# Kernel optimization log

Hardware: AMD Instinct MI355X
Metric: run time of the kernel (lower is better)

Reference implementation:

```python
import jax, jax.numpy as jnp
import numpy as np

KERNEL_MUL = 2.0
KERNEL_NUM = 5
EPS = 1e-3


def setup_inputs() -> dict:
    key = jax.random.key(0)
    k1, k2 = jax.random.split(key)
    source = jax.random.normal(k1, (2048, 512), dtype=jnp.float32)
    target = jax.random.normal(k2, (2048, 512), dtype=jnp.float32)
    beta = jnp.ones((KERNEL_NUM,), dtype=jnp.float32) / KERNEL_NUM
    return {"source": source, "target": target, "beta": beta}


def _sq_dists(total):
    # squared Euclidean pairwise distances, (N, N), clamped >= 0 (matches cdist(p=2)**2)
    sq = jnp.sum(total * total, axis=-1)
    d = sq[:, None] + sq[None, :] - 2.0 * (total @ total.T)
    return jnp.maximum(d, 0.0)


def _project_simplex(v):
    m = v.shape[0]
    mu = -jnp.sort(-v)                      # descending
    cs = jnp.cumsum(mu)
    ar = jnp.arange(1, m + 1, dtype=v.dtype)
    cond = mu - (cs - 1.0) / ar > 0
    idx = jnp.where(cond, jnp.arange(m), -1)
    rho = jnp.where(jnp.any(cond), jnp.max(idx), 0)
    theta = (cs[rho] - 1.0) / (rho + 1).astype(v.dtype)
    p = jnp.maximum(v - theta, 0.0)
    return p / (p.sum() + 1e-12)


def _update_beta(source, target, beta):
    # Batched version of the per-pair quad-kernel loop in _update_beta.
    Ns, D = source.shape
    Nt = target.shape[0]
    P = min(Ns // 2, Nt // 2)  # num_effective_pairs (static)
    s = source[: 2 * P].reshape(P, 2, D)
    t = target[: 2 * P].reshape(P, 2, D)
    quad = jnp.concatenate([s, t], axis=1)              # (P, 4, D) -> [s1, s2, t1, t2]
    diff = quad[:, :, None, :] - quad[:, None, :, :]
    sq = jnp.sum(diff * diff, axis=-1)                  # (P, 4, 4)
    offdiag = ~np.eye(4, dtype=bool)
    bw = jnp.median(sq[:, offdiag], axis=1) + 1e-6      # per-pair median of nonzero dists
    bw = bw / (KERNEL_MUL ** (KERNEL_NUM // 2))
    bws = bw[:, None] * (KERNEL_MUL ** jnp.arange(KERNEL_NUM, dtype=bw.dtype))[None, :]
    K = jnp.exp(-sq[:, None, :, :] / bws[:, :, None, None])   # (P, 5, 4, 4)
    g = K[:, :, 0, 1] + K[:, :, 2, 3] - K[:, :, 0, 2] - K[:, :, 1, 3]  # (P, 5)
    gm = jnp.mean(g, axis=0)
    Q = (g.T @ g) / P - jnp.outer(gm, gm) + EPS * jnp.eye(KERNEL_NUM, dtype=g.dtype)
    # projected gradient descent on the simplex (lr=1, max_iter=100, tol=1e-6)
    def cond_fn(st):
        _, _, i, conv = st
        return (i < 100) & (~conv)
    def body_fn(st):
        b, _, i, _ = st
        proj = _project_simplex(b - Q @ b)
        conv = jnp.linalg.norm(proj - b) < 1e-6
        return (proj, proj, i + 1, conv)
    _, proj, _, _ = jax.lax.while_loop(
        cond_fn, body_fn, (beta, beta, jnp.int32(0), jnp.array(False)))
    return proj


def _forward(source, target, beta):
    beta_new = _update_beta(jax.lax.stop_gradient(source),
                            jax.lax.stop_gradient(target), beta)
    Ns = source.shape[0]
    total = jnp.concatenate([source, target], axis=0)   # (N, D)
    N = total.shape[0]
    sq = _sq_dists(total)                               # (N, N)
    offdiag = ~np.eye(N, dtype=bool)
    bw = jnp.median(sq[offdiag]) + 1e-6
    bw = bw / (KERNEL_MUL ** (KERNEL_NUM // 2))
    bws = bw * (KERNEL_MUL ** jnp.arange(KERNEL_NUM, dtype=sq.dtype))  # (5,)
    Ks = jnp.exp(-sq[None, :, :] / bws[:, None, None])  # (5, N, N)
    joint = jnp.einsum('k,kij->ij', beta_new, Ks)
    XX = joint[:Ns, :Ns]
    YY = joint[Ns:, Ns:]
    XY = joint[:Ns, Ns:]
    n = XX.shape[0]
    m = YY.shape[0]
    term_XX = (jnp.sum(XX) - jnp.trace(XX)) / (n * (n - 1))
    term_YY = (jnp.sum(YY) - jnp.trace(YY)) / (m * (m - 1))
    term_XY = jnp.sum(XY) / (n * m)
    loss = term_XX + term_YY - 2.0 * term_XY
    return jnp.maximum(loss, 0.0)


def reference(source, target, beta):
    return _forward(source, target, beta)
```

## Files before the change

kernel.cpp:

```cpp
#include <hip/hip_runtime.h>
#include <math.h>

#define NT 4096
#define NS 2048
#define DDIM 512
#define KN 5
#define NTILES 528

typedef __bf16 bf16x8 __attribute__((ext_vector_type(8)));
typedef float f32x4 __attribute__((ext_vector_type(4)));
typedef unsigned short u16x8 __attribute__((ext_vector_type(8)));

static __device__ inline unsigned short f2bf(float x) {
    unsigned u = __float_as_uint(x);
    unsigned r = (u + 0x7fffu + ((u >> 16) & 1u)) >> 16;
    return (unsigned short)r;
}
static __device__ inline float bf2f(unsigned short h) {
    return __uint_as_float(((unsigned)h) << 16);
}

static __device__ inline void tri_map(int b, int& bx, int& by) {
    int x = (int)((sqrtf(8.0f * (float)b + 1.0f) - 1.0f) * 0.5f);
    while ((x + 1) * (x + 2) / 2 <= b) ++x;
    while (x * (x + 1) / 2 > b) --x;
    bx = x;
    by = b - x * (x + 1) / 2;
}

static __device__ void beta_solve(const float* __restrict__ g,
                                  const float* __restrict__ beta_in,
                                  float* __restrict__ beta_out)
{
    int lane = threadIdx.x;
    float gs[KN] = {0, 0, 0, 0, 0};
    float gg[15];
    #pragma unroll
    for (int i = 0; i < 15; ++i) gg[i] = 0.0f;
    for (int p = lane; p < 1024; p += 64) {
        float gv[KN];
        #pragma unroll
        for (int k = 0; k < KN; ++k) gv[k] = g[(size_t)p * KN + k];
        int idx = 0;
        #pragma unroll
        for (int a2 = 0; a2 < KN; ++a2) {
            gs[a2] += gv[a2];
            #pragma unroll
            for (int b2 = a2; b2 < KN; ++b2) gg[idx++] += gv[a2] * gv[b2];
        }
    }
    #pragma unroll
    for (int m = 32; m > 0; m >>= 1) {
        #pragma unroll
        for (int k = 0; k < KN; ++k) gs[k] += __shfl_xor(gs[k], m);
        #pragma unroll
        for (int i = 0; i < 15; ++i) gg[i] += __shfl_xor(gg[i], m);
    }
    if (lane != 0) return;

    float Q[KN][KN], gm[KN];
    #pragma unroll
    for (int k = 0; k < KN; ++k) gm[k] = gs[k] * (1.0f / 1024.0f);
    int idx = 0;
    #pragma unroll
    for (int a2 = 0; a2 < KN; ++a2)
        #pragma unroll
        for (int b2 = a2; b2 < KN; ++b2) {
            float qv = gg[idx++] * (1.0f / 1024.0f) - gm[a2] * gm[b2];
            Q[a2][b2] = qv; Q[b2][a2] = qv;
        }
    #pragma unroll
    for (int k = 0; k < KN; ++k) Q[k][k] += 0.001f;

    float b[KN], proj[KN];
    #pragma unroll
    for (int k = 0; k < KN; ++k) { b[k] = beta_in[k]; proj[k] = b[k]; }
    for (int it = 0; it < 100; ++it) {
        float v[KN];
        #pragma unroll
        for (int a2 = 0; a2 < KN; ++a2) {
            float qb = Q[a2][0] * b[0] + Q[a2][1] * b[1] + Q[a2][2] * b[2]
                     + Q[a2][3] * b[3] + Q[a2][4] * b[4];
            v[a2] = b[a2] - qb;
        }
        float mu0 = v[0], mu1 = v[1], mu2 = v[2], mu3 = v[3], mu4 = v[4];
#define CMPSW(x, y) { float hi_ = fmaxf(x, y); float lo_ = fminf(x, y); x = hi_; y = lo_; }
        CMPSW(mu0, mu1) CMPSW(mu3, mu4) CMPSW(mu2, mu4) CMPSW(mu2, mu3)
        CMPSW(mu0, mu3) CMPSW(mu0, mu2) CMPSW(mu1, mu4) CMPSW(mu1, mu3) CMPSW(mu1, mu2)
#undef CMPSW
        float cs0 = mu0, cs1 = cs0 + mu1, cs2 = cs1 + mu2, cs3 = cs2 + mu3, cs4 = cs3 + mu4;
        bool c1 = mu1 * 2.0f > cs1 - 1.0f;
        bool c2 = mu2 * 3.0f > cs2 - 1.0f;
        bool c3 = mu3 * 4.0f > cs3 - 1.0f;
        bool c4 = mu4 * 5.0f > cs4 - 1.0f;
        float csSel = cs0, rcpSel = 1.0f;
        if (c1) { csSel = cs1; rcpSel = 0.5f; }
        if (c2) { csSel = cs2; rcpSel = (1.0f / 3.0f); }
        if (c3) { csSel = cs3; rcpSel = 0.25f; }
        if (c4) { csSel = cs4; rcpSel = 0.2f; }
        float theta = (csSel - 1.0f) * rcpSel;
        float ssum = 0.0f;
        #pragma unroll
        for (int k = 0; k < KN; ++k) { proj[k] = fmaxf(v[k] - theta, 0.0f); ssum += proj[k]; }
        float invs = 1.0f / (ssum + 1e-12f);
        float nd = 0.0f;
        #pragma unroll
        for (int k = 0; k < KN; ++k) {
            proj[k] *= invs;
            float dd = proj[k] - b[k];
            nd += dd * dd;
            b[k] = proj[k];
        }
        if (nd < 1e-12f) break;
    }
    #pragma unroll
    for (int k = 0; k < KN; ++k) beta_out[k] = proj[k];
}

__global__ __launch_bounds__(256) void k_prep2(const float* __restrict__ S,
                                               const float* __restrict__ T,
                                               unsigned short* __restrict__ Hi,
                                               unsigned short* __restrict__ Lo,
                                               float* __restrict__ norms,
                                               float* __restrict__ g,
                                               unsigned* __restrict__ hists,
                                               unsigned* __restrict__ sel)
{
    if (blockIdx.x < 44) hists[blockIdx.x * 256 + threadIdx.x] = 0;
    if (blockIdx.x == 50 && threadIdx.x == 0) {
        sel[0] = 0u; sel[1] = 8386559u;
        sel[2] = 0u; sel[3] = 8386560u;
    }
    int p = blockIdx.x * 4 + (threadIdx.x >> 6);
    int l = threadIdx.x & 63;
    const float* r0 = S + (size_t)(2 * p) * DDIM;
    const float* r1 = r0 + DDIM;
    const float* r2 = T + (size_t)(2 * p) * DDIM;
    const float* r3 = r2 + DDIM;
    float a[8], b[8], c[8], d[8];
    *(float4*)&a[0] = *(const float4*)(r0 + l * 8); *(float4*)&a[4] = *(const float4*)(r0 + l * 8 + 4);
    *(float4*)&b[0] = *(const float4*)(r1 + l * 8); *(float4*)&b[4] = *(const float4*)(r1 + l * 8 + 4);
    *(float4*)&c[0] = *(const float4*)(r2 + l * 8); *(float4*)&c[4] = *(const float4*)(r2 + l * 8 + 4);
    *(float4*)&d[0] = *(const float4*)(r3 + l * 8); *(float4*)&d[4] = *(const float4*)(r3 + l * 8 + 4);

    float n0 = 0, n1 = 0, n2 = 0, n3 = 0;
    float s01 = 0, s23 = 0, s02 = 0, s13 = 0, s03 = 0, s12 = 0;
    u16x8 h0, l0, h1, l1, h2, l2, h3, l3;
    #pragma unroll
    for (int k = 0; k < 8; ++k) {
        float va = a[k], vb = b[k], vc = c[k], vd = d[k];
        n0 += va * va; n1 += vb * vb; n2 += vc * vc; n3 += vd * vd;
        float t01 = va - vb, t23 = vc - vd, t02 = va - vc, t13 = vb - vd;
        s01 += t01*t01; s23 += t23*t23; s02 += t02*t02; s13 += t13*t13;
        float t03 = va - vd, t12 = vb - vc;
        s03 += t03*t03; s12 += t12*t12;
        unsigned short hh;
        hh = f2bf(va); h0[k] = hh; l0[k] = f2bf(va - bf2f(hh));
        hh = f2bf(vb); h1[k] = hh; l1[k] = f2bf(vb - bf2f(hh));
        hh = f2bf(vc); h2[k] = hh; l2[k] = f2bf(vc - bf2f(hh));
        hh = f2bf(vd); h3[k] = hh; l3[k] = f2bf(vd - bf2f(hh));
    }
    size_t g0 = (size_t)(2 * p) * DDIM + l * 8;
    size_t g1 = g0 + DDIM;
    size_t g2 = (size_t)(NS + 2 * p) * DDIM + l * 8;
    size_t g3 = g2 + DDIM;
    *(u16x8*)&Hi[g0] = h0; *(u16x8*)&Lo[g0] = l0;
    *(u16x8*)&Hi[g1] = h1; *(u16x8*)&Lo[g1] = l1;
    *(u16x8*)&Hi[g2] = h2; *(u16x8*)&Lo[g2] = l2;
    *(u16x8*)&Hi[g3] = h3; *(u16x8*)&Lo[g3] = l3;

    #pragma unroll
    for (int m = 32; m > 0; m >>= 1) {
        n0 += __shfl_xor(n0, m); n1 += __shfl_xor(n1, m);
        n2 += __shfl_xor(n2, m); n3 += __shfl_xor(n3, m);
        s01 += __shfl_xor(s01, m); s23 += __shfl_xor(s23, m);
        s02 += __shfl_xor(s02, m); s13 += __shfl_xor(s13, m);
        s03 += __shfl_xor(s03, m); s12 += __shfl_xor(s12, m);
    }
    if (l == 0) {
        norms[2 * p] = n0; norms[2 * p + 1] = n1;
        norms[NS + 2 * p] = n2; norms[NS + 2 * p + 1] = n3;
        float v[6] = { s01, s02, s03, s12, s13, s23 };
        for (int i = 0; i < 5; ++i)
            for (int j = 0; j < 5 - i; ++j)
                if (v[j] > v[j + 1]) { float t = v[j]; v[j] = v[j + 1]; v[j + 1] = t; }
        float med = 0.5f * (v[2] + v[3]);
        float bw = (med + 1e-6f) * 0.25f;
        #pragma unroll
        for (int k = 0; k < KN; ++k) {
            float inv = 1.0f / (bw * (float)(1 << k));
            g[(size_t)p * KN + k] = expf(-s01 * inv) + expf(-s23 * inv)
                                  - expf(-s02 * inv) - expf(-s13 * inv);
        }
    }
}

__global__ __launch_bounds__(256) void k_dist_mfma(const unsigned short* __restrict__ Hi,
                                                   const unsigned short* __restrict__ Lo,
                                                   const float* __restrict__ norms,
                                                   float* __restrict__ D,
                                                   const float* __restrict__ g,
                                                   const float* __restrict__ beta_in,
                                                   float* __restrict__ beta_out)
{
    __shared__ __align__(16) unsigned short sA[2][2][128][32];
    __shared__ __align__(16) unsigned short sB[2][2][128][32];

    if (blockIdx.x == 0) {
        if (threadIdx.x < 64) beta_solve(g, beta_in, beta_out);
        return;
    }

    int bb = blockIdx.x - 1;
    int swz = (bb & 7) * 66 + (bb >> 3);
    int bx, by;
    tri_map(swz, bx, by);
    const int m0 = by * 128, n0 = bx * 128;

    const int tid = threadIdx.x;
    const int w = tid >> 6, l = tid & 63;
    const int wr = w >> 1, wc = w & 1;

    const int chunk = (l & 3) ^ ((((l >> 2) & 3) + ((l >> 4) & 3)) & 3);
    const size_t gA0 = (size_t)(m0 + w * 16 + (l >> 2)) * DDIM + chunk * 8;
    const size_t gA1 = gA0 + (size_t)64 * DDIM;
    const size_t gB0 = (size_t)(n0 + w * 16 + (l >> 2)) * DDIM + chunk * 8;
    const size_t gB1 = gB0 + (size_t)64 * DDIM;
    const unsigned w1024 = w * 1024;

#define GLD(dst, srcptr, goff)                                                      \
    __builtin_amdgcn_global_load_lds(                                               \
        (const __attribute__((address_space(1))) unsigned*)((srcptr) + (goff)),     \
        (__attribute__((address_space(3))) unsigned*)((char*)(dst) + w1024), 16, 0, 0)
#define STAGE(buf, kk)                                  \
    do {                                                \
        GLD(&sA[buf][0][0][0],  Hi, gA0 + (kk));        \
        GLD(&sA[buf][0][64][0], Hi, gA1 + (kk));        \
        GLD(&sA[buf][1][0][0],  Lo, gA0 + (kk));        \
        GLD(&sA[buf][1][64][0], Lo, gA1 + (kk));        \
        GLD(&sB[buf][0][0][0],  Hi, gB0 + (kk));        \
        GLD(&sB[buf][0][64][0], Hi, gB1 + (kk));        \
        GLD(&sB[buf][1][0][0],  Lo, gB0 + (kk));        \
        GLD(&sB[buf][1][64][0], Lo, gB1 + (kk));        \
    } while (0)

    f32x4 acc[4][4] = {};
    const int q = l >> 4;
    const int fr = ((l & 3) + ((l >> 2) & 3)) & 3;
    const unsigned soff = ((unsigned)(q ^ fr)) << 4;
    const unsigned rowbA = (wr * 64 + (l & 15)) * 64 + soff;
    const unsigned rowbB = (wc * 64 + (l & 15)) * 64 + soff;

    STAGE(0, 0);
    __syncthreads();

    #pragma unroll 2
    for (int t = 0; t < 16; ++t) {
        const int cur = t & 1;
        if (t < 15) STAGE(cur ^ 1, (t + 1) * 32);

        bf16x8 ah[4], al[4], bh[4], bl[4];
        #pragma unroll
        for (int m = 0; m < 4; ++m) {
            ah[m] = *(const bf16x8*)((const char*)&sA[cur][0][0][0] + rowbA + m * 1024);
            al[m] = *(const bf16x8*)((const char*)&sA[cur][1][0][0] + rowbA + m * 1024);
        }
        #pragma unroll
        for (int n = 0; n < 4; ++n) {
            bh[n] = *(const bf16x8*)((const char*)&sB[cur][0][0][0] + rowbB + n * 1024);
            bl[n] = *(const bf16x8*)((const char*)&sB[cur][1][0][0] + rowbB + n * 1024);
        }
        #pragma unroll
        for (int m = 0; m < 4; ++m)
            #pragma unroll
            for (int n = 0; n < 4; ++n) {
                acc[m][n] = __builtin_amdgcn_mfma_f32_16x16x32_bf16(bh[n], ah[m], acc[m][n], 0, 0, 0);
                acc[m][n] = __builtin_amdgcn_mfma_f32_16x16x32_bf16(bl[n], ah[m], acc[m][n], 0, 0, 0);
                acc[m][n] = __builtin_amdgcn_mfma_f32_16x16x32_bf16(bh[n], al[m], acc[m][n], 0, 0, 0);
            }
        __syncthreads();
    }
#undef STAGE
#undef GLD

    float* rowbuf = (float*)&sA[0][0][0][0] + w * 1024;
    const int rr = l & 15;
    #pragma unroll
    for (int m = 0; m < 4; ++m) {
        float nrm = norms[m0 + wr * 64 + m * 16 + rr];
        #pragma unroll
        for (int n = 0; n < 4; ++n) {
            int cb = n0 + wc * 64 + n * 16 + (q << 2);
            float4 ncv = *(const float4*)&norms[cb];
            f32x4 a = acc[m][n];
            float4 o;
            o.x = fmaxf(nrm + ncv.x - 2.0f * a[0], 0.0f);
            o.y = fmaxf(nrm + ncv.y - 2.0f * a[1], 0.0f);
            o.z = fmaxf(nrm + ncv.z - 2.0f * a[2], 0.0f);
            o.w = fmaxf(nrm + ncv.w - 2.0f * a[3], 0.0f);
            int ch = (n * 4 + q) ^ (rr & 7);
            *(float4*)(rowbuf + rr * 64 + ch * 4) = o;
        }
        #pragma unroll
        for (int s = 0; s < 4; ++s) {
            int row = s * 4 + q;
            int ch = (l & 15) ^ (row & 7);
            float4 v = *(const float4*)(rowbuf + row * 64 + ch * 4);
            *(float4*)&D[(size_t)(m0 + wr * 64 + m * 16 + row) * NT + n0 + wc * 64 + (l & 15) * 4] = v;
        }
    }
}

__global__ __launch_bounds__(256) void k_hist0_tri(const float* __restrict__ D,
                                                   unsigned* __restrict__ gH)
{
    __shared__ unsigned h[1024];
    for (int i = threadIdx.x; i < 1024; i += 256) h[i] = 0;
    int bx, by;
    tri_map(blockIdx.x, bx, by);
    int m0 = by * 128, n0 = bx * 128;
    unsigned wt = (bx != by) ? 2u : 1u;
    __syncthreads();
    for (int v = threadIdx.x; v < 4096; v += 256) {
        int r = m0 + (v >> 5);
        int c0 = n0 + (v & 31) * 4;
        float4 dv = *(const float4*)&D[(size_t)r * NT + c0];
        const float* dd = (const float*)&dv;
        unsigned pb = __float_as_uint(dd[0]) >> 22;
        unsigned pc = (r == c0) ? 0u : wt;
        #pragma unroll
        for (int j = 1; j < 4; ++j) {
            unsigned bj = __float_as_uint(dd[j]) >> 22;
            unsigned cj = (r == c0 + j) ? 0u : wt;
            if (bj == pb) pc += cj;
            else {
                if (pc) atomicAdd(&h[pb], pc);
                pb = bj; pc = cj;
            }
        }
        if (pc) atomicAdd(&h[pb], pc);
    }
    __syncthreads();
    for (int i = threadIdx.x; i < 1024; i += 256) {
        unsigned c = h[i];
        if (c) atomicAdd(&gH[i], c);
    }
}

__global__ __launch_bounds__(64) void k_scan0(const unsigned* __restrict__ hL0,
                                              unsigned* __restrict__ sel)
{
    int lane = threadIdx.x;
    for (int t = 0; t < 2; ++t) {
        unsigned r = sel[t * 2 + 1];
        unsigned s = 0;
        for (int i = 0; i < 16; ++i) s += hL0[lane * 16 + i];
        unsigned x = s;
        #pragma unroll
        for (int off = 1; off < 64; off <<= 1) {
            unsigned y = __shfl_up(x, off);
            if (lane >= off) x += y;
        }
        unsigned base = x - s;
        bool has = (r >= base) && (r < base + s);
        unsigned long long mm = __ballot(has);
        int leader = __ffsll(mm) - 1;
        unsigned bin = 0, cb = 0;
        if (lane == leader) {
            unsigned cc = base;
            for (int i = 0; i < 16; ++i) {
                unsigned hv = hL0[lane * 16 + i];
                if (r < cc + hv) { bin = lane * 16 + i; cb = cc; break; }
                cc += hv;
            }
        }
        bin = __shfl(bin, leader);
        cb = __shfl(cb, leader);
        if (lane == 0) {
            sel[t * 2 + 0] = bin;
            sel[t * 2 + 1] = r - cb;
        }
    }
}

template<int LEVEL>
__global__ __launch_bounds__(256) void k_hist_tri(const float* __restrict__ D,
                                                  const unsigned* __restrict__ sel,
                                                  unsigned* __restrict__ gA,
                                                  unsigned* __restrict__ gB)
{
    constexpr int NB = (LEVEL == 2) ? 4096 : 1024;
    __shared__ unsigned lha[NB];
    __shared__ unsigned lhb[NB];
    for (int i = threadIdx.x; i < NB; i += 256) { lha[i] = 0; lhb[i] = 0; }
    unsigned pA = sel[0], pB = sel[2];
    int bx, by;
    tri_map(blockIdx.x, bx, by);
    int m0 = by * 128, n0 = bx * 128;
    unsigned wt = (bx != by) ? 2u : 1u;
    __syncthreads();
    for (int v = threadIdx.x; v < 4096; v += 256) {
        int r = m0 + (v >> 5);
        int c0 = n0 + (v & 31) * 4;
        float4 dv = *(const float4*)&D[(size_t)r * NT + c0];
        const float* dd = (const float*)&dv;
        #pragma unroll
        for (int j = 0; j < 4; ++j) {
            if (r == c0 + j) continue;
            unsigned key = __float_as_uint(dd[j]);
            if constexpr (LEVEL == 1) {
                if ((key >> 22) == pA) atomicAdd(&lha[(key >> 12) & 1023], wt);
                if ((key >> 22) == pB) atomicAdd(&lhb[(key >> 12) & 1023], wt);
            } else {
                if ((key >> 12) == pA) atomicAdd(&lha[key & 4095], wt);
                if ((key >> 12) == pB) atomicAdd(&lhb[key & 4095], wt);
            }
        }
    }
    __syncthreads();
    for (int i = threadIdx.x; i < NB; i += 256) {
        unsigned ca = lha[i];
        if (ca) atomicAdd(&gA[i], ca);
        unsigned cb = lhb[i];
        if (cb) atomicAdd(&gB[i], cb);
    }
}

template<int LEVEL>
__global__ __launch_bounds__(64) void k_scan(const unsigned* __restrict__ hA,
                                             const unsigned* __restrict__ hB,
                                             unsigned* __restrict__ sel,
                                             float* __restrict__ params)
{
    constexpr int NB = (LEVEL == 2) ? 4096 : 1024;
    constexpr int C = NB / 64;
    int lane = threadIdx.x;
    for (int t = 0; t < 2; ++t) {
        const unsigned* h = (t == 0 ? hA : hB);
        unsigned r = sel[t * 2 + 1];
        unsigned s = 0;
        for (int i = 0; i < C; ++i) s += h[lane * C + i];
        unsigned x = s;
        #pragma unroll
        for (int off = 1; off < 64; off <<= 1) {
            unsigned y = __shfl_up(x, off);
            if (lane >= off) x += y;
        }
        unsigned base = x - s;
        bool has = (r >= base) && (r < base + s);
        unsigned long long mm = __ballot(has);
        int leader = __ffsll(mm) - 1;
        unsigned bin = 0, cb = 0;
        if (lane == leader) {
            unsigned cc = base;
            for (int i = 0; i < C; ++i) {
                unsigned hv = h[lane * C + i];
                if (r < cc + hv) { bin = lane * C + i; cb = cc; break; }
                cc += hv;
            }
        }
        bin = __shfl(bin, leader);
        cb = __shfl(cb, leader);
        if (lane == 0) {
            if (LEVEL == 1) sel[t * 2 + 0] = (sel[t * 2 + 0] << 10) | bin;
            else            sel[4 + t]     = (sel[t * 2 + 0] << 12) | bin;
            sel[t * 2 + 1] = r - cb;
        }
    }
    if (LEVEL == 2 && lane == 0) {
        float vA = __uint_as_float(sel[4]);
        float vB = __uint_as_float(sel[5]);
        float med = 0.5f * (vA + vB);
        float bw = (med + 1e-6f) * 0.25f;
        #pragma unroll
        for (int k = 0; k < KN; ++k) params[k] = 1.0f / (bw * (float)(1 << k));
    }
}

__global__ __launch_bounds__(256) void k_wsum_tri(const float* __restrict__ D,
                                                  const float* __restrict__ params,
                                                  const float* __restrict__ beta,
                                                  double* __restrict__ partials)
{
    float i0 = params[0], i1 = params[1], i2 = params[2], i3 = params[3], i4 = params[4];
    float b0 = beta[0], b1 = beta[1], b2 = beta[2], b3 = beta[3], b4 = beta[4];
    const double wDiag = 1.0 / ((double)NS * (NS - 1));
    const double wOff = -1.0 / ((double)NS * NS);
    int bx, by;
    tri_map(blockIdx.x, bx, by);
    int m0 = by * 128, n0 = bx * 128;
    double wt = (bx != by) ? 2.0 : 1.0;
    double acc = 0.0;
    for (int v = threadIdx.x; v < 4096; v += 256) {
        int r = m0 + (v >> 5);
        int c0 = n0 + (v & 31) * 4;
        float4 dv = *(const float4*)&D[(size_t)r * NT + c0];
        const float* dd = (const float*)&dv;
        #pragma unroll
        for (int j = 0; j < 4; ++j) {
            int c = c0 + j;
            if (r == c) continue;
            float sq = dd[j];
            float val = b0 * __expf(-sq * i0) + b1 * __expf(-sq * i1) + b2 * __expf(-sq * i2)
                      + b3 * __expf(-sq * i3) + b4 * __expf(-sq * i4);
            bool same = (r < NS) == (c < NS);
            acc += (same ? wDiag : wOff) * (double)val;
        }
    }
    acc *= wt;
    __shared__ double red[256];
    red[threadIdx.x] = acc;
    __syncthreads();
    for (int off = 128; off > 0; off >>= 1) {
        if (threadIdx.x < off) red[threadIdx.x] += red[threadIdx.x + off];
        __syncthreads();
    }
    if (threadIdx.x == 0) partials[blockIdx.x] = red[0];
}

__global__ __launch_bounds__(256) void k_final(const double* __restrict__ partials,
                                               float* __restrict__ out, int count)
{
    double acc = 0;
    for (int i = threadIdx.x; i < count; i += 256) acc += partials[i];
    __shared__ double red[256];
    red[threadIdx.x] = acc;
    __syncthreads();
    for (int off = 128; off > 0; off >>= 1) {
        if (threadIdx.x < off) red[threadIdx.x] += red[threadIdx.x + off];
        __syncthreads();
    }
    if (threadIdx.x == 0) out[0] = (float)fmax(red[0], 0.0);
}

extern "C" void kernel_launch(void* const* d_in, const int* in_sizes, int n_in,
                              void* d_out, int out_size, void* d_ws, size_t ws_size,
                              hipStream_t stream)
{
    const float* S = (const float*)d_in[0];
    const float* T = (const float*)d_in[1];
    const float* beta = (const float*)d_in[2];
    float* out = (float*)d_out;

    float* D = (float*)d_ws;
    unsigned short* Hi = (unsigned short*)(D + (size_t)NT * NT);
    unsigned short* Lo = Hi + (size_t)NT * DDIM;
    float* norms = (float*)(Lo + (size_t)NT * DDIM);
    float* g = norms + NT;
    float* beta2 = g + 1024 * KN;
    float* params = beta2 + 8;
    unsigned* sel = (unsigned*)(params + 8);
    unsigned* hists = sel + 16;
    unsigned* hL0 = hists;
    unsigned* hL1A = hL0 + 1024;
    unsigned* hL1B = hL1A + 1024;
    unsigned* hL2A = hL1B + 1024;
    unsigned* hL2B = hL2A + 4096;
    double* partials = (double*)(hists + 11264);

    k_prep2<<<dim3(256), dim3(256), 0, stream>>>(S, T, Hi, Lo, norms, g, hists, sel);
    k_dist_mfma<<<dim3(NTILES + 1), dim3(256), 0, stream>>>(Hi, Lo, norms, D, g, beta, beta2);
    k_hist0_tri<<<dim3(NTILES), dim3(256), 0, stream>>>(D, hL0);
    k_scan0<<<dim3(1), dim3(64), 0, stream>>>(hL0, sel);
    k_hist_tri<1><<<dim3(NTILES), dim3(256), 0, stream>>>(D, sel, hL1A, hL1B);
    k_scan<1><<<dim3(1), dim3(64), 0, stream>>>(hL1A, hL1B, sel, params);
    k_hist_tri<2><<<dim3(NTILES), dim3(256), 0, stream>>>(D, sel, hL2A, hL2B);
    k_scan<2><<<dim3(1), dim3(64), 0, stream>>>(hL2A, hL2B, sel, params);
    k_wsum_tri<<<dim3(NTILES), dim3(256), 0, stream>>>(D, params, beta2, partials);
    k_final<<<dim3(1), dim3(256), 0, stream>>>(partials, out, NTILES);
}
```

Before: 151.7 us.

## Enlarge distance GEMM tiles to 256x128 to raise operand reuse

The MFMA distance kernel now computes 256x128 output tiles (4 warps, each 64x128) instead of 128x128, cutting the block count from 528 to 272 over the upper triangle. Each loaded B fragment is reused across twice as many rows, and the epilogue reads norms from an LDS cache. Diagonal blocks skip storing the lower half. The cost is doubled accumulators per thread (launch_bounds 256,1), which lowers occupancy and register headroom, and fewer blocks for 256 CUs.

Result: slower. 174.7 us (+15.2%).

```diff
diff --git a/kernel.cpp b/kernel.cpp
--- a/kernel.cpp
+++ b/kernel.cpp
@@ -6,6 +6,7 @@
 #define DDIM 512
 #define KN 5
 #define NTILES 528
+#define NDBLK 272
 
 typedef __bf16 bf16x8 __attribute__((ext_vector_type(8)));
 typedef float f32x4 __attribute__((ext_vector_type(4)));
@@ -195,15 +196,15 @@
     }
 }
 
-__global__ __launch_bounds__(256) void k_dist_mfma(const unsigned short* __restrict__ Hi,
-                                                   const unsigned short* __restrict__ Lo,
-                                                   const float* __restrict__ norms,
-                                                   float* __restrict__ D,
-                                                   const float* __restrict__ g,
-                                                   const float* __restrict__ beta_in,
-                                                   float* __restrict__ beta_out)
-{
-    __shared__ __align__(16) unsigned short sA[2][2][128][32];
+__global__ __launch_bounds__(256, 1) void k_dist_mfma(const unsigned short* __restrict__ Hi,
+                                                      const unsigned short* __restrict__ Lo,
+                                                      const float* __restrict__ norms,
+                                                      float* __restrict__ D,
+                                                      const float* __restrict__ g,
+                                                      const float* __restrict__ beta_in,
+                                                      float* __restrict__ beta_out)
+{
+    __shared__ __align__(16) unsigned short sA[2][2][256][32];
     __shared__ __align__(16) unsigned short sB[2][2][128][32];
 
     if (blockIdx.x == 0) {
@@ -212,101 +213,122 @@
     }
 
     int bb = blockIdx.x - 1;
-    int swz = (bb & 7) * 66 + (bb >> 3);
-    int bx, by;
-    tri_map(swz, bx, by);
-    const int m0 = by * 128, n0 = bx * 128;
+    int swz = (bb & 7) * 34 + (bb >> 3);
+    int t2 = swz, R = 0;
+    while (t2 >= 32 - 2 * R) { t2 -= 32 - 2 * R; ++R; }
+    const int C = 2 * R + t2;
+    const int m0 = R * 256, n0 = C * 128;
+    const bool diag = (C == 2 * R);
 
     const int tid = threadIdx.x;
     const int w = tid >> 6, l = tid & 63;
-    const int wr = w >> 1, wc = w & 1;
-
-    const int chunk = (l & 3) ^ ((((l >> 2) & 3) + ((l >> 4) & 3)) & 3);
-    const size_t gA0 = (size_t)(m0 + w * 16 + (l >> 2)) * DDIM + chunk * 8;
-    const size_t gA1 = gA0 + (size_t)64 * DDIM;
-    const size_t gB0 = (size_t)(n0 + w * 16 + (l >> 2)) * DDIM + chunk * 8;
-    const size_t gB1 = gB0 + (size_t)64 * DDIM;
-    const unsigned w1024 = w * 1024;
+
+    const int chunk = (tid & 3) ^ ((((tid >> 2) & 3) + ((tid >> 4) & 3)) & 3);
+    const int srow = tid >> 2;
+    size_t gA[4], gB[2];
+    #pragma unroll
+    for (int rb = 0; rb < 4; ++rb) gA[rb] = (size_t)(m0 + rb * 64 + srow) * DDIM + chunk * 8;
+    #pragma unroll
+    for (int rb = 0; rb < 2; ++rb) gB[rb] = (size_t)(n0 + rb * 64 + srow) * DDIM + chunk * 8;
+    const unsigned wbase = w * 1024;
 
 #define GLD(dst, srcptr, goff)                                                      \
     __builtin_amdgcn_global_load_lds(                                               \
         (const __attribute__((address_space(1))) unsigned*)((srcptr) + (goff)),     \
-        (__attribute__((address_space(3))) unsigned*)((char*)(dst) + w1024), 16, 0, 0)
-#define STAGE(buf, kk)                                  \
-    do {                                                \
-        GLD(&sA[buf][0][0][0],  Hi, gA0 + (kk));        \
-        GLD(&sA[buf][0][64][0], Hi, gA1 + (kk));        \
-        GLD(&sA[buf][1][0][0],  Lo, gA0 + (kk));        \
-        GLD(&sA[buf][1][64][0], Lo, gA1 + (kk));        \
-        GLD(&sB[buf][0][0][0],  Hi, gB0 + (kk));        \
-        GLD(&sB[buf][0][64][0], Hi, gB1 + (kk));        \
-        GLD(&sB[buf][1][0][0],  Lo, gB0 + (kk));        \
-        GLD(&sB[buf][1][64][0], Lo, gB1 + (kk));        \
+        (__attribute__((address_space(3))) unsigned*)((char*)(dst) + wbase), 16, 0, 0)
+#define STAGE(buf, kk)                                       \
+    do {                                                     \
+        GLD(&sA[buf][0][0][0],   Hi, gA[0] + (kk));          \
+        GLD(&sA[buf][0][64][0],  Hi, gA[1] + (kk));          \
+        GLD(&sA[buf][0][128][0], Hi, gA[2] + (kk));          \
+        GLD(&sA[buf][0][192][0], Hi, gA[3] + (kk));          \
+        GLD(&sA[buf][1][0][0],   Lo, gA[0] + (kk));          \
+        GLD(&sA[buf][1][64][0],  Lo, gA[1] + (kk));          \
+        GLD(&sA[buf][1][128][0], Lo, gA[2] + (kk));          \
+        GLD(&sA[buf][1][192][0], Lo, gA[3] + (kk));          \
+        GLD(&sB[buf][0][0][0],   Hi, gB[0] + (kk));          \
+        GLD(&sB[buf][0][64][0],  Hi, gB[1] + (kk));          \
+        GLD(&sB[buf][1][0][0],   Lo, gB[0] + (kk));          \
+        GLD(&sB[buf][1][64][0],  Lo, gB[1] + (kk));          \
     } while (0)
 
-    f32x4 acc[4][4] = {};
+    f32x4 acc[4][8] = {};
     const int q = l >> 4;
     const int fr = ((l & 3) + ((l >> 2) & 3)) & 3;
     const unsigned soff = ((unsigned)(q ^ fr)) << 4;
-    const unsigned rowbA = (wr * 64 + (l & 15)) * 64 + soff;
-    const unsigned rowbB = (wc * 64 + (l & 15)) * 64 + soff;
+    const unsigned rowA = (w * 64 + (l & 15)) * 64 + soff;
+    const unsigned rowB = (l & 15) * 64 + soff;
 
     STAGE(0, 0);
     __syncthreads();
 
-    #pragma unroll 2
     for (int t = 0; t < 16; ++t) {
         const int cur = t & 1;
         if (t < 15) STAGE(cur ^ 1, (t + 1) * 32);
 
-        bf16x8 ah[4], al[4], bh[4], bl[4];
+        bf16x8 ah[4], al[4];
         #pragma unroll
         for (int m = 0; m < 4; ++m) {
-            ah[m] = *(const bf16x8*)((const char*)&sA[cur][0][0][0] + rowbA + m * 1024);
-            al[m] = *(const bf16x8*)((const char*)&sA[cur][1][0][0] + rowbA + m * 1024);
-        }
-        #pragma unroll
-        for (int n = 0; n < 4; ++n) {
-            bh[n] = *(const bf16x8*)((const char*)&sB[cur][0][0][0] + rowbB + n * 1024);
-            bl[n] = *(const bf16x8*)((const char*)&sB[cur][1][0][0] + rowbB + n * 1024);
-        }
-        #pragma unroll
-        for (int m = 0; m < 4; ++m)
+            ah[m] = *(const bf16x8*)((const char*)&sA[cur][0][0][0] + rowA + m * 1024);
+            al[m] = *(const bf16x8*)((const char*)&sA[cur][1][0][0] + rowA + m * 1024);
+        }
+        #pragma unroll
+        for (int half = 0; half < 2; ++half) {
+            bf16x8 bh[4], bl[4];
             #pragma unroll
             for (int n = 0; n < 4; ++n) {
-                acc[m][n] = __builtin_amdgcn_mfma_f32_16x16x32_bf16(bh[n], ah[m], acc[m][n], 0, 0, 0);
-                acc[m][n] = __builtin_amdgcn_mfma_f32_16x16x32_bf16(bl[n], ah[m], acc[m][n], 0, 0, 0);
-                acc[m][n] = __builtin_amdgcn_mfma_f32_16x16x32_bf16(bh[n], al[m], acc[m][n], 0, 0, 0);
+                bh[n] = *(const bf16x8*)((const char*)&sB[cur][0][0][0] + rowB + (half * 4 + n) * 1024);
+                bl[n] = *(const bf16x8*)((const char*)&sB[cur][1][0][0] + rowB + (half * 4 + n) * 1024);
             }
+            #pragma unroll
+            for (int m = 0; m < 4; ++m)
+                #pragma unroll
+                for (int n = 0; n < 4; ++n) {
+                    int nn = half * 4 + n;
+                    acc[m][nn] = __builtin_amdgcn_mfma_f32_16x16x32_bf16(bh[n], ah[m], acc[m][nn], 0, 0, 0);
+                    acc[m][nn] = __builtin_amdgcn_mfma_f32_16x16x32_bf16(bl[n], ah[m], acc[m][nn], 0, 0, 0);
+                    acc[m][nn] = __builtin_amdgcn_mfma_f32_16x16x32_bf16(bh[n], al[m], acc[m][nn], 0, 0, 0);
+                }
+        }
         __syncthreads();
     }
 #undef STAGE
 #undef GLD
 
-    float* rowbuf = (float*)&sA[0][0][0][0] + w * 1024;
+    float* ncache = (float*)&sB[0][0][0][0];
+    ncache[tid] = norms[m0 + tid];
+    if (tid < 128) ncache[256 + tid] = norms[n0 + tid];
+    __syncthreads();
+
+    if (diag && w >= 2) return;
+
+    float* rowbuf = (float*)&sA[0][0][0][0] + w * 2048;
     const int rr = l & 15;
     #pragma unroll
     for (int m = 0; m < 4; ++m) {
-        float nrm = norms[m0 + wr * 64 + m * 16 + rr];
-        #pragma unroll
-        for (int n = 0; n < 4; ++n) {
-            int cb = n0 + wc * 64 + n * 16 + (q << 2);
-            float4 ncv = *(const float4*)&norms[cb];
+        float nrm = ncache[w * 64 + m * 16 + rr];
+        #pragma unroll
+        for (int n = 0; n < 8; ++n) {
+            float4 ncv = *(const float4*)&ncache[256 + n * 16 + (q << 2)];
             f32x4 a = acc[m][n];
             float4 o;
             o.x = fmaxf(nrm + ncv.x - 2.0f * a[0], 0.0f);
             o.y = fmaxf(nrm + ncv.y - 2.0f * a[1], 0.0f);
             o.z = fmaxf(nrm + ncv.z - 2.0f * a[2], 0.0f);
             o.w = fmaxf(nrm + ncv.w - 2.0f * a[3], 0.0f);
-            int ch = (n * 4 + q) ^ (rr & 7);
-            *(float4*)(rowbuf + rr * 64 + ch * 4) = o;
+            int cw = (n * 4 + q) ^ (rr & 7);
+            *(float4*)(rowbuf + rr * 128 + cw * 4) = o;
         }
         #pragma unroll
         for (int s = 0; s < 4; ++s) {
             int row = s * 4 + q;
-            int ch = (l & 15) ^ (row & 7);
-            float4 v = *(const float4*)(rowbuf + row * 64 + ch * 4);
-            *(float4*)&D[(size_t)(m0 + wr * 64 + m * 16 + row) * NT + n0 + wc * 64 + (l & 15) * 4] = v;
+            #pragma unroll
+            for (int h = 0; h < 2; ++h) {
+                int c = h * 16 + (l & 15);
+                int cr = c ^ (row & 7);
+                float4 v = *(const float4*)(rowbuf + row * 128 + cr * 4);
+                *(float4*)&D[(size_t)(m0 + w * 64 + m * 16 + row) * NT + n0 + c * 4] = v;
+            }
         }
     }
 }
@@ -552,14 +574,14 @@
     unsigned* sel = (unsigned*)(params + 8);
     unsigned* hists = sel + 16;
     unsigned* hL0 = hists;
-    unsigned* hL1A = hL0 + 1024;
-    unsigned* hL1B = hL1A + 1024;
-    unsigned* hL2A = hL1B + 1024;
-    unsigned* hL2B = hL2A + 4096;
+    unsigned* hL1A = hists + 1024;
+    unsigned* hL1B = hists + 2048;
+    unsigned* hL2A = hists + 3072;
+    unsigned* hL2B = hists + 7168;
     double* partials = (double*)(hists + 11264);
 
     k_prep2<<<dim3(256), dim3(256), 0, stream>>>(S, T, Hi, Lo, norms, g, hists, sel);
-    k_dist_mfma<<<dim3(NTILES + 1), dim3(256), 0, stream>>>(Hi, Lo, norms, D, g, beta, beta2);
+    k_dist_mfma<<<dim3(NDBLK + 1), dim3(256), 0, stream>>>(Hi, Lo, norms, D, g, beta, beta2);
     k_hist0_tri<<<dim3(NTILES), dim3(256), 0, stream>>>(D, hL0);
     k_scan0<<<dim3(1), dim3(64), 0, stream>>>(hL0, sel);
     k_hist_tri<1><<<dim3(NTILES), dim3(256), 0, stream>>>(D, sel, hL1A, hL1B);
```

## Fuse level-0 histogram into distance GEMM epilogue and final reduction into wsum

Applied to the files above, without the earlier changes.

Builds the first radix-select histogram inside the distance kernel's epilogue, using per-wave shared-memory histograms fed from the values just written. This removes a separate full pass over the distance matrix. It also folds the final partial-sum reduction into the weighted-sum kernel with a last-block atomic ticket, removing one launch. In exchange the GEMM epilogue gets extra LDS atomics and shared-memory reuse, and the ticket counter now has to be zeroed by the prep kernel.

New measurement: 152.6 us. Within noise of the previous version (+0.6%).

```diff
diff --git a/kernel.cpp b/kernel.cpp
--- a/kernel.cpp
+++ b/kernel.cpp
@@ -126,7 +126,7 @@
                                                unsigned* __restrict__ hists,
                                                unsigned* __restrict__ sel)
 {
-    if (blockIdx.x < 44) hists[blockIdx.x * 256 + threadIdx.x] = 0;
+    if (blockIdx.x < 45) hists[blockIdx.x * 256 + threadIdx.x] = 0;
     if (blockIdx.x == 50 && threadIdx.x == 0) {
         sel[0] = 0u; sel[1] = 8386559u;
         sel[2] = 0u; sel[3] = 8386560u;
@@ -201,7 +201,8 @@
                                                    float* __restrict__ D,
                                                    const float* __restrict__ g,
                                                    const float* __restrict__ beta_in,
-                                                   float* __restrict__ beta_out)
+                                                   float* __restrict__ beta_out,
+                                                   unsigned* __restrict__ gH)
 {
     __shared__ __align__(16) unsigned short sA[2][2][128][32];
     __shared__ __align__(16) unsigned short sB[2][2][128][32];
@@ -283,15 +284,23 @@
 #undef STAGE
 #undef GLD
 
+    float* ncache = (float*)&sB[0][0][0][0];
+    unsigned* hrep = (unsigned*)&sB[0][0][0][0] + 256;
+    if (tid < 128) ncache[tid] = norms[m0 + tid];
+    else           ncache[tid] = norms[n0 + tid - 128];
+    for (int i = tid; i < 4096; i += 256) hrep[i] = 0;
+    __syncthreads();
+
+    unsigned* hmine = hrep + w * 1024;
+    const unsigned wgt = (bx != by) ? 2u : 1u;
     float* rowbuf = (float*)&sA[0][0][0][0] + w * 1024;
     const int rr = l & 15;
     #pragma unroll
     for (int m = 0; m < 4; ++m) {
-        float nrm = norms[m0 + wr * 64 + m * 16 + rr];
+        float nrm = ncache[wr * 64 + m * 16 + rr];
         #pragma unroll
         for (int n = 0; n < 4; ++n) {
-            int cb = n0 + wc * 64 + n * 16 + (q << 2);
-            float4 ncv = *(const float4*)&norms[cb];
+            float4 ncv = *(const float4*)&ncache[128 + wc * 64 + n * 16 + (q << 2)];
             f32x4 a = acc[m][n];
             float4 o;
             o.x = fmaxf(nrm + ncv.x - 2.0f * a[0], 0.0f);
@@ -306,43 +315,27 @@
             int row = s * 4 + q;
             int ch = (l & 15) ^ (row & 7);
             float4 v = *(const float4*)(rowbuf + row * 64 + ch * 4);
-            *(float4*)&D[(size_t)(m0 + wr * 64 + m * 16 + row) * NT + n0 + wc * 64 + (l & 15) * 4] = v;
-        }
-    }
-}
-
-__global__ __launch_bounds__(256) void k_hist0_tri(const float* __restrict__ D,
-                                                   unsigned* __restrict__ gH)
-{
-    __shared__ unsigned h[1024];
-    for (int i = threadIdx.x; i < 1024; i += 256) h[i] = 0;
-    int bx, by;
-    tri_map(blockIdx.x, bx, by);
-    int m0 = by * 128, n0 = bx * 128;
-    unsigned wt = (bx != by) ? 2u : 1u;
-    __syncthreads();
-    for (int v = threadIdx.x; v < 4096; v += 256) {
-        int r = m0 + (v >> 5);
-        int c0 = n0 + (v & 31) * 4;
-        float4 dv = *(const float4*)&D[(size_t)r * NT + c0];
-        const float* dd = (const float*)&dv;
-        unsigned pb = __float_as_uint(dd[0]) >> 22;
-        unsigned pc = (r == c0) ? 0u : wt;
-        #pragma unroll
-        for (int j = 1; j < 4; ++j) {
-            unsigned bj = __float_as_uint(dd[j]) >> 22;
-            unsigned cj = (r == c0 + j) ? 0u : wt;
-            if (bj == pb) pc += cj;
-            else {
-                if (pc) atomicAdd(&h[pb], pc);
-                pb = bj; pc = cj;
-            }
-        }
-        if (pc) atomicAdd(&h[pb], pc);
-    }
-    __syncthreads();
-    for (int i = threadIdx.x; i < 1024; i += 256) {
-        unsigned c = h[i];
+            int rowg = m0 + wr * 64 + m * 16 + row;
+            int colg = n0 + wc * 64 + (l & 15) * 4;
+            *(float4*)&D[(size_t)rowg * NT + colg] = v;
+            unsigned b0_ = __float_as_uint(v.x) >> 22;
+            unsigned b1_ = __float_as_uint(v.y) >> 22;
+            unsigned b2_ = __float_as_uint(v.z) >> 22;
+            unsigned b3_ = __float_as_uint(v.w) >> 22;
+            unsigned pb = b0_, pc = (rowg == colg) ? 0u : wgt;
+            unsigned cj;
+            cj = (rowg == colg + 1) ? 0u : wgt;
+            if (b1_ == pb) pc += cj; else { if (pc) atomicAdd(&hmine[pb], pc); pb = b1_; pc = cj; }
+            cj = (rowg == colg + 2) ? 0u : wgt;
+            if (b2_ == pb) pc += cj; else { if (pc) atomicAdd(&hmine[pb], pc); pb = b2_; pc = cj; }
+            cj = (rowg == colg + 3) ? 0u : wgt;
+            if (b3_ == pb) pc += cj; else { if (pc) atomicAdd(&hmine[pb], pc); pb = b3_; pc = cj; }
+            if (pc) atomicAdd(&hmine[pb], pc);
+        }
+    }
+    __syncthreads();
+    for (int i = tid; i < 1024; i += 256) {
+        unsigned c = hrep[i] + hrep[i + 1024] + hrep[i + 2048] + hrep[i + 3072];
         if (c) atomicAdd(&gH[i], c);
     }
 }
@@ -477,11 +470,15 @@
     }
 }
 
-__global__ __launch_bounds__(256) void k_wsum_tri(const float* __restrict__ D,
-                                                  const float* __restrict__ params,
-                                                  const float* __restrict__ beta,
-                                                  double* __restrict__ partials)
-{
+__global__ __launch_bounds__(256) void k_wsumf(const float* __restrict__ D,
+                                               const float* __restrict__ params,
+                                               const float* __restrict__ beta,
+                                               double* __restrict__ partials,
+                                               unsigned* __restrict__ cnt,
+                                               float* __restrict__ out)
+{
+    __shared__ double red[256];
+    __shared__ unsigned tk;
     float i0 = params[0], i1 = params[1], i2 = params[2], i3 = params[3], i4 = params[4];
     float b0 = beta[0], b1 = beta[1], b2 = beta[2], b3 = beta[3], b4 = beta[4];
     const double wDiag = 1.0 / ((double)NS * (NS - 1));
@@ -508,29 +505,33 @@
         }
     }
     acc *= wt;
-    __shared__ double red[256];
     red[threadIdx.x] = acc;
     __syncthreads();
     for (int off = 128; off > 0; off >>= 1) {
         if (threadIdx.x < off) red[threadIdx.x] += red[threadIdx.x + off];
         __syncthreads();
     }
-    if (threadIdx.x == 0) partials[blockIdx.x] = red[0];
-}
-
-__global__ __launch_bounds__(256) void k_final(const double* __restrict__ partials,
-                                               float* __restrict__ out, int count)
-{
-    double acc = 0;
-    for (int i = threadIdx.x; i < count; i += 256) acc += partials[i];
-    __shared__ double red[256];
-    red[threadIdx.x] = acc;
-    __syncthreads();
-    for (int off = 128; off > 0; off >>= 1) {
-        if (threadIdx.x < off) red[threadIdx.x] += red[threadIdx.x + off];
+    if (threadIdx.x == 0) {
+        partials[blockIdx.x] = red[0];
+        __threadfence();
+        tk = atomicAdd(&cnt[0], 1u);
+    }
+    __syncthreads();
+    if (tk == NTILES - 1) {
+        __threadfence();
+        double a2 = 0.0;
+        for (int i = threadIdx.x; i < NTILES; i += 256) {
+            unsigned long long u = atomicAdd((unsigned long long*)&partials[i], 0ull);
+            a2 += __longlong_as_double(u);
+        }
+        red[threadIdx.x] = a2;
         __syncthreads();
-    }
-    if (threadIdx.x == 0) out[0] = (float)fmax(red[0], 0.0);
+        for (int off = 128; off > 0; off >>= 1) {
+            if (threadIdx.x < off) red[threadIdx.x] += red[threadIdx.x + off];
+            __syncthreads();
+        }
+        if (threadIdx.x == 0) out[0] = (float)fmax(red[0], 0.0);
+    }
 }
 
 extern "C" void kernel_launch(void* const* d_in, const int* in_sizes, int n_in,
@@ -552,20 +553,19 @@
     unsigned* sel = (unsigned*)(params + 8);
     unsigned* hists = sel + 16;
     unsigned* hL0 = hists;
-    unsigned* hL1A = hL0 + 1024;
-    unsigned* hL1B = hL1A + 1024;
-    unsigned* hL2A = hL1B + 1024;
-    unsigned* hL2B = hL2A + 4096;
-    double* partials = (double*)(hists + 11264);
+    unsigned* hL1A = hists + 1024;
+    unsigned* hL1B = hists + 2048;
+    unsigned* hL2A = hists + 3072;
+    unsigned* hL2B = hists + 7168;
+    unsigned* cnt  = hists + 11264;
+    double* partials = (double*)(hists + 11520);
 
     k_prep2<<<dim3(256), dim3(256), 0, stream>>>(S, T, Hi, Lo, norms, g, hists, sel);
-    k_dist_mfma<<<dim3(NTILES + 1), dim3(256), 0, stream>>>(Hi, Lo, norms, D, g, beta, beta2);
-    k_hist0_tri<<<dim3(NTILES), dim3(256), 0, stream>>>(D, hL0);
+    k_dist_mfma<<<dim3(NTILES + 1), dim3(256), 0, stream>>>(Hi, Lo, norms, D, g, beta, beta2, hL0);
     k_scan0<<<dim3(1), dim3(64), 0, stream>>>(hL0, sel);
     k_hist_tri<1><<<dim3(NTILES), dim3(256), 0, stream>>>(D, sel, hL1A, hL1B);
     k_scan<1><<<dim3(1), dim3(64), 0, stream>>>(hL1A, hL1B, sel, params);
     k_hist_tri<2><<<dim3(NTILES), dim3(256), 0, stream>>>(D, sel, hL2A, hL2B);
     k_scan<2><<<dim3(1), dim3(64), 0, stream>>>(hL2A, hL2B, sel, params);
-    k_wsum_tri<<<dim3(NTILES), dim3(256), 0, stream>>>(D, params, beta2, partials);
-    k_final<<<dim3(1), dim3(256), 0, stream>>>(partials, out, NTILES);
-}
+    k_wsumf<<<dim3(NTILES), dim3(256), 0, stream>>>(D, params, beta2, partials, cnt, out);
+}
```

## Match XCD tile swizzle across passes, cache norms in LDS, derive exps by squaring

Applied to the files above, without the earlier changes.

The histogram and weighted-sum passes now use the same XCD-aware tile mapping as the distance kernel. The intent is that each tile of D is reread on the chiplet whose L2 likely still holds it. The distance epilogue stages the row and column norms in shared memory instead of issuing repeated global loads. The weighted sum computes one exp for the widest bandwidth and gets the other four kernels by repeated squaring, which relies on the bandwidths being exact powers of two apart and may change rounding slightly.

Measured after the change: 144.4 us (median of 2 runs). 1.05x faster.

```diff
diff --git a/kernel.cpp b/kernel.cpp
--- a/kernel.cpp
+++ b/kernel.cpp
@@ -26,6 +26,10 @@
     while (x * (x + 1) / 2 > b) --x;
     bx = x;
     by = b - x * (x + 1) / 2;
+}
+
+static __device__ inline int xcd_tile(int bb) {
+    return (bb & 7) * 66 + (bb >> 3);
 }
 
 static __device__ void beta_solve(const float* __restrict__ g,
@@ -211,10 +215,8 @@
         return;
     }
 
-    int bb = blockIdx.x - 1;
-    int swz = (bb & 7) * 66 + (bb >> 3);
     int bx, by;
-    tri_map(swz, bx, by);
+    tri_map(xcd_tile(blockIdx.x - 1), bx, by);
     const int m0 = by * 128, n0 = bx * 128;
 
     const int tid = threadIdx.x;
@@ -283,15 +285,19 @@
 #undef STAGE
 #undef GLD
 
+    float* ncache = (float*)&sB[0][0][0][0];
+    if (tid < 128) ncache[tid] = norms[m0 + tid];
+    else           ncache[tid] = norms[n0 + tid - 128];
+    __syncthreads();
+
     float* rowbuf = (float*)&sA[0][0][0][0] + w * 1024;
     const int rr = l & 15;
     #pragma unroll
     for (int m = 0; m < 4; ++m) {
-        float nrm = norms[m0 + wr * 64 + m * 16 + rr];
+        float nrm = ncache[wr * 64 + m * 16 + rr];
         #pragma unroll
         for (int n = 0; n < 4; ++n) {
-            int cb = n0 + wc * 64 + n * 16 + (q << 2);
-            float4 ncv = *(const float4*)&norms[cb];
+            float4 ncv = *(const float4*)&ncache[128 + wc * 64 + n * 16 + (q << 2)];
             f32x4 a = acc[m][n];
             float4 o;
             o.x = fmaxf(nrm + ncv.x - 2.0f * a[0], 0.0f);
@@ -314,10 +320,11 @@
 __global__ __launch_bounds__(256) void k_hist0_tri(const float* __restrict__ D,
                                                    unsigned* __restrict__ gH)
 {
+    if (blockIdx.x == 0) return;
     __shared__ unsigned h[1024];
     for (int i = threadIdx.x; i < 1024; i += 256) h[i] = 0;
     int bx, by;
-    tri_map(blockIdx.x, bx, by);
+    tri_map(xcd_tile(blockIdx.x - 1), bx, by);
     int m0 = by * 128, n0 = bx * 128;
     unsigned wt = (bx != by) ? 2u : 1u;
     __syncthreads();
@@ -389,13 +396,14 @@
                                                   unsigned* __restrict__ gA,
                                                   unsigned* __restrict__ gB)
 {
+    if (blockIdx.x == 0) return;
     constexpr int NB = (LEVEL == 2) ? 4096 : 1024;
     __shared__ unsigned lha[NB];
     __shared__ unsigned lhb[NB];
     for (int i = threadIdx.x; i < NB; i += 256) { lha[i] = 0; lhb[i] = 0; }
     unsigned pA = sel[0], pB = sel[2];
     int bx, by;
-    tri_map(blockIdx.x, bx, by);
+    tri_map(xcd_tile(blockIdx.x - 1), bx, by);
     int m0 = by * 128, n0 = bx * 128;
     unsigned wt = (bx != by) ? 2u : 1u;
     __syncthreads();
@@ -482,12 +490,13 @@
                                                   const float* __restrict__ beta,
                                                   double* __restrict__ partials)
 {
-    float i0 = params[0], i1 = params[1], i2 = params[2], i3 = params[3], i4 = params[4];
+    if (blockIdx.x == 0) { if (threadIdx.x == 0) partials[NTILES] = 0.0; return; }
+    float i4 = params[4];
     float b0 = beta[0], b1 = beta[1], b2 = beta[2], b3 = beta[3], b4 = beta[4];
     const double wDiag = 1.0 / ((double)NS * (NS - 1));
     const double wOff = -1.0 / ((double)NS * NS);
     int bx, by;
-    tri_map(blockIdx.x, bx, by);
+    tri_map(xcd_tile(blockIdx.x - 1), bx, by);
     int m0 = by * 128, n0 = bx * 128;
     double wt = (bx != by) ? 2.0 : 1.0;
     double acc = 0.0;
@@ -501,8 +510,12 @@
             int c = c0 + j;
             if (r == c) continue;
             float sq = dd[j];
-            float val = b0 * __expf(-sq * i0) + b1 * __expf(-sq * i1) + b2 * __expf(-sq * i2)
-                      + b3 * __expf(-sq * i3) + b4 * __expf(-sq * i4);
+            float y1 = __expf(-sq * i4);
+            float y2 = y1 * y1;
+            float y4 = y2 * y2;
+            float y8 = y4 * y4;
+            float y16 = y8 * y8;
+            float val = b4 * y1 + b3 * y2 + b2 * y4 + b1 * y8 + b0 * y16;
             bool same = (r < NS) == (c < NS);
             acc += (same ? wDiag : wOff) * (double)val;
         }
@@ -515,7 +528,7 @@
         if (threadIdx.x < off) red[threadIdx.x] += red[threadIdx.x + off];
         __syncthreads();
     }
-    if (threadIdx.x == 0) partials[blockIdx.x] = red[0];
+    if (threadIdx.x == 0) partials[blockIdx.x - 1] = red[0];
 }
 
 __global__ __launch_bounds__(256) void k_final(const double* __restrict__ partials,
@@ -552,20 +565,20 @@
     unsigned* sel = (unsigned*)(params + 8);
     unsigned* hists = sel + 16;
     unsigned* hL0 = hists;
-    unsigned* hL1A = hL0 + 1024;
-    unsigned* hL1B = hL1A + 1024;
-    unsigned* hL2A = hL1B + 1024;
-    unsigned* hL2B = hL2A + 4096;
+    unsigned* hL1A = hists + 1024;
+    unsigned* hL1B = hists + 2048;
+    unsigned* hL2A = hists + 3072;
+    unsigned* hL2B = hists + 7168;
     double* partials = (double*)(hists + 11264);
 
     k_prep2<<<dim3(256), dim3(256), 0, stream>>>(S, T, Hi, Lo, norms, g, hists, sel);
     k_dist_mfma<<<dim3(NTILES + 1), dim3(256), 0, stream>>>(Hi, Lo, norms, D, g, beta, beta2);
-    k_hist0_tri<<<dim3(NTILES), dim3(256), 0, stream>>>(D, hL0);
+    k_hist0_tri<<<dim3(NTILES + 1), dim3(256), 0, stream>>>(D, hL0);
     k_scan0<<<dim3(1), dim3(64), 0, stream>>>(hL0, sel);
-    k_hist_tri<1><<<dim3(NTILES), dim3(256), 0, stream>>>(D, sel, hL1A, hL1B);
+    k_hist_tri<1><<<dim3(NTILES + 1), dim3(256), 0, stream>>>(D, sel, hL1A, hL1B);
     k_scan<1><<<dim3(1), dim3(64), 0, stream>>>(hL1A, hL1B, sel, params);
-    k_hist_tri<2><<<dim3(NTILES), dim3(256), 0, stream>>>(D, sel, hL2A, hL2B);
+    k_hist_tri<2><<<dim3(NTILES + 1), dim3(256), 0, stream>>>(D, sel, hL2A, hL2B);
     k_scan<2><<<dim3(1), dim3(64), 0, stream>>>(hL2A, hL2B, sel, params);
-    k_wsum_tri<<<dim3(NTILES), dim3(256), 0, stream>>>(D, params, beta2, partials);
+    k_wsum_tri<<<dim3(NTILES + 1), dim3(256), 0, stream>>>(D, params, beta2, partials);
     k_final<<<dim3(1), dim3(256), 0, stream>>>(partials, out, NTILES);
 }
```
